# Optimization experiments

Measured on AMD Instinct MI355X. Metric: run time of the kernel, lower is better.

Reference implementation:

```python
import jax, jax.numpy as jnp
import numpy as np

B, L1, L2, D1, D2, H, P = 32, 256, 64, 256, 256, 256, 128
I = D1 + D2  # gate / GRU input dim


def setup_inputs() -> dict:
    key = jax.random.key(0)
    ks = jax.random.split(key, 10)
    s = 0.05  # weight init scale
    return {
        "sequence1": jax.random.normal(ks[0], (B, L1, D1), jnp.float32),
        "sequence2": jax.random.normal(ks[1], (B, L2, D2), jnp.float32),
        "sequence1_mask": jnp.ones((B, L1), jnp.float32),
        "sequence2_mask": jnp.ones((B, L2), jnp.float32),
        "W1": jax.random.normal(ks[2], (D2, P), jnp.float32) * s,
        "W2": jax.random.normal(ks[3], (D1 + H, P), jnp.float32) * s,
        "v": jax.random.normal(ks[4], (P,), jnp.float32) * s,
        "Wg": jax.random.normal(ks[5], (I, I), jnp.float32) * s,
        "bg": jnp.zeros((I,), jnp.float32),
        "w_ih": jax.random.normal(ks[6], (3 * H, I), jnp.float32) * s,
        "w_hh": jax.random.normal(ks[7], (3 * H, H), jnp.float32) * s,
        "b_ih": jnp.zeros((3 * H,), jnp.float32),
        "b_hh": jnp.zeros((3 * H,), jnp.float32),
    }


def reference(sequence1, sequence2, sequence1_mask, sequence2_mask,
              W1, W2, v, Wg, bg, w_ih, w_hh, b_ih, b_hh):
    # Precompute sequence2 projection once: [B, L2, P]
    seq2_proj = jnp.einsum('bld,dp->blp', sequence2, W1)
    # Additive mask for softmax over L2
    neg = jnp.where(sequence2_mask > 0, 0.0, -1e9)  # [B, L2]
    xs = jnp.transpose(sequence1, (1, 0, 2))  # [L1, B, D1]

    def step(h, x_t):
        # attention: v^T tanh(W1*seq2_j + W2*[x_t; h])
        vec = jnp.concatenate([x_t, h], axis=-1)            # [B, D1+H]
        s = jnp.einsum('blp,p->bl',
                       jnp.tanh(seq2_proj + (vec @ W2)[:, None, :]), v) + neg
        w = jax.nn.softmax(s, axis=-1)                      # [B, L2]
        att = jnp.einsum('bl,bld->bd', w, sequence2)        # [B, D2]
        inp = jnp.concatenate([x_t, att], axis=-1)          # [B, I]
        # gated attention: sigmoid(Linear(inp)) * inp
        inp = jax.nn.sigmoid(inp @ Wg.T + bg) * inp
        # GRUCell (torch semantics)
        gi = inp @ w_ih.T + b_ih
        gh = h @ w_hh.T + b_hh
        ir, iz, inn = jnp.split(gi, 3, axis=-1)
        hr, hz, hn = jnp.split(gh, 3, axis=-1)
        r = jax.nn.sigmoid(ir + hr)
        z = jax.nn.sigmoid(iz + hz)
        n = jnp.tanh(inn + r * hn)
        h_new = (1.0 - z) * n + z * h
        return h_new, h_new

    h0 = jnp.zeros((sequence1.shape[0], w_hh.shape[1]), sequence1.dtype)
    _, hs = jax.lax.scan(step, h0, xs)                      # [L1, B, H]
    out = jnp.transpose(hs, (1, 0, 2)) * sequence1_mask[:, :, None]
    return out
```

## Files before the change

### kernel.cpp

```cpp
#include <hip/hip_runtime.h>

typedef _Float16 half2_v __attribute__((ext_vector_type(2)));
typedef unsigned int u32;

#define W2K_O    0
#define WHHP_O   16384
#define WIHP_O   114688
#define NPACKW   311296
#define S2P_B    1245184
#define S2T_B    1769472
#define M1_B     2818048
#define PROJX_B  4915200
#define GATEX_B  7012352
#define EXCH_B   15400960

#define SMEM_BYTES 156928

__device__ __forceinline__ float fdot2(half2_v a, half2_v b, float c) {
    return __builtin_amdgcn_fdot2(a, b, c, false);
}
__device__ __forceinline__ half2_v h2_of(u32 u) { return __builtin_bit_cast(half2_v, u); }
__device__ __forceinline__ u32 pack_h2(float a, float b) {
    half2_v r; r[0] = (_Float16)a; r[1] = (_Float16)b;
    return __builtin_bit_cast(u32, r);
}
__device__ __forceinline__ float dot4(uint4 w, uint4 a, float acc) {
    acc = fdot2(h2_of(w.x), h2_of(a.x), acc);
    acc = fdot2(h2_of(w.y), h2_of(a.y), acc);
    acc = fdot2(h2_of(w.z), h2_of(a.z), acc);
    acc = fdot2(h2_of(w.w), h2_of(a.w), acc);
    return acc;
}
__device__ __forceinline__ float fast_tanh(float x) {
    float e = __expf(2.0f * x);
    return 1.0f - 2.0f / (e + 1.0f);
}
__device__ __forceinline__ float fast_sigmoid(float x) {
    return 1.0f / (1.0f + __expf(-x));
}
__device__ __forceinline__ u32 aload(const u32* p) {
    return __hip_atomic_load(p, __ATOMIC_RELAXED, __HIP_MEMORY_SCOPE_AGENT);
}
__device__ __forceinline__ void astore(u32* p, u32 v) {
    __hip_atomic_store(p, v, __ATOMIC_RELAXED, __HIP_MEMORY_SCOPE_AGENT);
}
__device__ __forceinline__ u32 mkw(float x, u32 st) {
    unsigned short hb = __builtin_bit_cast(unsigned short, (_Float16)x);
    return (st << 16) | (u32)hb;
}
__device__ __forceinline__ float f16low(u32 v) {
    return (float)__builtin_bit_cast(_Float16, (unsigned short)(v & 0xFFFFu));
}

__global__ void prep_pack_w(const float* __restrict__ W2, const float* __restrict__ wih,
                            const float* __restrict__ whh, u32* __restrict__ ws_u) {
    int idx = blockIdx.x * 256 + threadIdx.x;
    if (idx >= NPACKW) return;
    float a, c;
    if (idx < WHHP_O) {
        int mm = idx >> 11, r = idx & 2047, p = r >> 4, kl = r & 15;
        int row = 256 + mm * 32 + 2 * kl;
        a = W2[row * 128 + p]; c = W2[(row + 1) * 128 + p];
    } else if (idx < WIHP_O) {
        int t2 = idx - WHHP_O, mm = t2 / 12288, r = t2 % 12288, o = r >> 7, k = r & 127;
        int row = (o >> 5) * 256 + mm * 32 + (o & 31);
        a = whh[row * 256 + 2 * k]; c = whh[row * 256 + 2 * k + 1];
    } else {
        int t2 = idx - WIHP_O, mm = t2 / 24576, r = t2 % 24576, o = r >> 8, k = r & 255;
        int row = (o >> 5) * 256 + mm * 32 + (o & 31);
        a = wih[row * 512 + 2 * k]; c = wih[row * 512 + 2 * k + 1];
    }
    ws_u[idx] = pack_h2(a, c);
}

__global__ void prep_s2p(const float* __restrict__ seq2, const float* __restrict__ W1,
                         _Float16* __restrict__ outh) {
    int idx = blockIdx.x * 256 + threadIdx.x;
    int p = idx & 127, j = (idx >> 7) & 63, b = idx >> 13;
    const float* s2 = seq2 + (b * 64 + j) * 256;
    float acc = 0.f;
    #pragma unroll 8
    for (int d = 0; d < 256; ++d) acc += s2[d] * W1[d * 128 + p];
    outh[idx] = (_Float16)acc;
}

__global__ void prep_s2T(const float* __restrict__ seq2, _Float16* __restrict__ dst) {
    int idx = blockIdx.x * 256 + threadIdx.x;
    int j = idx & 63, d = (idx >> 6) & 255, b = idx >> 14;
    dst[idx] = (_Float16)seq2[(b * 64 + j) * 256 + d];
}

__global__ void prep_m1(const float* __restrict__ Wg, const float* __restrict__ seq2,
                        _Float16* __restrict__ dst) {
    int idx = blockIdx.x * 256 + threadIdx.x;
    int j = idx & 63, o = (idx >> 6) & 511, b = idx >> 15;
    const float* wr = Wg + o * 512 + 256;
    const float* s2 = seq2 + (b * 64 + j) * 256;
    float acc = 0.f;
    #pragma unroll 8
    for (int d = 0; d < 256; ++d) acc += wr[d] * s2[d];
    dst[idx] = (_Float16)acc;
}

__global__ void prep_gemm(const float* __restrict__ A, const float* __restrict__ Bsrc,
                          int mode, _Float16* __restrict__ C, int N) {
    __shared__ float As[64][17];
    __shared__ float Bs[16][65];
    int r0 = blockIdx.x * 64, n0 = blockIdx.y * 64;
    int tid = threadIdx.x;
    int tr = tid >> 4, tc = tid & 15;
    float acc[4][4] = {};
    for (int k0 = 0; k0 < 256; k0 += 16) {
        #pragma unroll
        for (int i = 0; i < 4; ++i) {
            int rr = (tid >> 4) + i * 16, kk = tid & 15;
            As[rr][kk] = A[(r0 + rr) * 256 + k0 + kk];
        }
        #pragma unroll
        for (int i = 0; i < 4; ++i) {
            if (mode == 0) { int kk = (tid >> 6) + i * 4, nn = tid & 63; Bs[kk][nn] = Bsrc[(k0 + kk) * N + n0 + nn]; }
            else           { int nn = (tid >> 4) + i * 16, kk = tid & 15; Bs[kk][nn] = Bsrc[(n0 + nn) * 512 + k0 + kk]; }
        }
        __syncthreads();
        #pragma unroll
        for (int k = 0; k < 16; ++k)
            #pragma unroll
            for (int i = 0; i < 4; ++i)
                #pragma unroll
                for (int j = 0; j < 4; ++j)
                    acc[i][j] += As[tr * 4 + i][k] * Bs[k][tc * 4 + j];
        __syncthreads();
    }
    for (int i = 0; i < 4; ++i)
        for (int j = 0; j < 4; ++j)
            C[(size_t)(r0 + tr * 4 + i) * N + n0 + tc * 4 + j] = (_Float16)acc[i][j];
}

__global__ void __launch_bounds__(1024) match_rnn(
    const float* __restrict__ seq1, const float* __restrict__ mask1,
    const float* __restrict__ mask2, const float* __restrict__ v,
    const float* __restrict__ bg, const float* __restrict__ bih,
    const float* __restrict__ bhh, char* __restrict__ ws, float* __restrict__ out)
{
    const int m = blockIdx.x >> 5;
    const int b = blockIdx.x & 31;
    const int tid = threadIdx.x;

    extern __shared__ char smem[];
    u32* s_whh4 = (u32*)smem;
    u32* s_wih4 = s_whh4 + 12288;
    u32* s_w2k  = s_wih4 + 12288;
    unsigned short* s_s2p = (unsigned short*)(s_w2k + 2176);
    u32* s_m1u  = (u32*)(s_s2p + 9216);
    u32* s_s2Tu = s_m1u + 2112;
    float* s_php = (float*)(s_s2Tu + 2112);
    float* s_red = s_php + 1024;
    u32* s_h2u  = (u32*)(s_red + 896);
    u32* s_ip2a = s_h2u + 160;
    u32* s_ip2b = s_ip2a + 160;
    float* s_projh = (float*)(s_ip2b + 160);
    float* s_projx = s_projh + 128;
    float* s_v   = s_projx + 128;
    float* s_w   = s_v + 128;
    float* s_neg = s_w + 64;
    float* s_gx  = s_neg + 64;
    float* s_xc  = s_gx + 64;
    float* s_bg  = s_xc + 64;
    float* s_sg  = s_bg + 64;
    float* s_attl = s_sg + 64;
    float* s_bih = s_attl + 64;
    float* s_bhh = s_bih + 96;
    float* s_gh  = s_bhh + 96;
    float* s_hf  = s_gh + 96;
    u32* s_hloc  = (u32*)(s_hf + 32);
    float* s_m1v = (float*)(s_hloc + 16);

    unsigned short* s_h2h  = (unsigned short*)s_h2u;
    unsigned short* s_ip2ah = (unsigned short*)s_ip2a;
    unsigned short* s_ip2bh = (unsigned short*)s_ip2b;

    const u32* wsrc = (const u32*)ws;

    for (int i = tid; i < 12288; i += 1024) {
        int o = i >> 7, k = i & 127, u = k >> 2;
        int du4 = ((o >> 3) * 256) + ((u & 3) * 64) + (((o & 7) << 3) | (u >> 2));
        s_whh4[du4 * 4 + (k & 3)] = wsrc[WHHP_O + m * 12288 + i];
    }
    for (int i = tid; i < 12288; i += 1024) {
        int o = i >> 7, k = i & 127, u = k >> 2;
        int du4 = ((o >> 3) * 256) + ((u & 3) * 64) + (((o & 7) << 3) | (u >> 2));
        s_wih4[du4 * 4 + (k & 3)] = wsrc[WIHP_O + m * 24576 + o * 256 + k];
    }
    for (int i = tid; i < 2048; i += 1024) {
        int p = i >> 4, kl = i & 15;
        s_w2k[p * 17 + kl] = wsrc[W2K_O + m * 2048 + i];
    }
    {
        const u32* s2src = wsrc + (S2P_B / 4) + b * 4096;
        for (int i = tid; i < 4096; i += 1024) {
            int j = i >> 6, kk = i & 63;
            ((u32*)s_s2p)[j * 72 + kk] = s2src[i];
        }
        const u32* m1src = wsrc + (M1_B / 4) + (b * 512 + m * 64) * 32;
        for (int i = tid; i < 2048; i += 1024) {
            int o = i >> 5, jw = i & 31;
            s_m1u[o * 33 + jw] = m1src[i];
        }
        if (m >= 4) {
            const u32* stsrc = wsrc + (S2T_B / 4) + (b * 256 + (m - 4) * 64) * 32;
            for (int i = tid; i < 2048; i += 1024) {
                int dd = i >> 5, jw = i & 31;
                s_s2Tu[dd * 33 + jw] = stsrc[i];
            }
        }
    }
    if (tid < 128) s_v[tid] = v[tid];
    if (tid < 64) { s_neg[tid] = (mask2[b * 64 + tid] > 0.f) ? 0.f : -1e9f; s_bg[tid] = bg[m * 64 + tid]; }
    if (tid < 96) {
        int row = (tid >> 5) * 256 + m * 32 + (tid & 31);
        s_bih[tid] = bih[row]; s_bhh[tid] = bhh[row];
    }
    if (tid < 32) s_hf[tid] = 0.f;

    uint4 wiA = {}, wiB = {}, wiC = {}, wiD = {};
    const int oAD = ((tid >> 6) << 3) + ((tid & 63) >> 3);
    const int ksAD = tid & 7;
    if (tid < 768) {
        const uint4* wip = (const uint4*)(wsrc + WIHP_O + m * 24576 + oAD * 256 + 128 + ksAD * 16);
        wiA = wip[0]; wiB = wip[1]; wiC = wip[2]; wiD = wip[3];
    }

    u32* exch = (u32*)(ws + EXCH_B) + b * 2048;
    const u32* g_projx = (const u32*)(ws + PROJX_B);
    const u32* g_gatex = (const u32*)(ws + GATEX_B);

    int dead = 0;
    __syncthreads();

    for (int t = 0; t < 256; ++t) {
        const u32 st = (u32)(t + 1);
        float4 xv = {};
        u32 pxv = 0, gxv = 0; float mkv = 0.f;
        if (tid >= 896 && tid < 912) {
            if (m < 4)
                xv = ((const float4*)(seq1 + (size_t)(b * 256 + t) * 256 + m * 64))[tid - 896];
        } else if (tid >= 912 && tid < 976)
            pxv = g_projx[(b * 256 + t) * 64 + (tid - 912)];
        else if (tid >= 976 && tid < 1008)
            gxv = g_gatex[(b * 256 + t) * 256 + m * 32 + (tid - 976)];
        else if (tid == 1008)
            mkv = mask1[b * 256 + t];

        if (t > 0) {
            u32 v1, v2;
            const bool p2 = tid < 256;
            const u32 stp = (u32)t;
            if (!dead) {
                int sp = 0;
                for (;;) {
                    v1 = aload(exch + tid);
                    v2 = p2 ? aload(exch + 1024 + tid) : (stp << 16);
                    bool ok = ((v1 >> 16) == stp) && ((v2 >> 16) == stp);
                    if (__all((int)ok)) break;
                    __builtin_amdgcn_s_sleep(1);
                    if (++sp > (1 << 17)) { dead = 1; break; }
                }
            } else { v1 = aload(exch + tid); v2 = p2 ? aload(exch + 1024 + tid) : 0; }
            { int mm = tid >> 7, p = tid & 127; s_php[p * 8 + mm] = f16low(v1); }
            if (p2) {
                int k = tid;
                int pos = ((k >> 5) * 20 + ((k >> 1) & 15)) * 2 + (k & 1);
                s_h2h[pos] = (unsigned short)(v2 & 0xFFFFu);
            }
        } else {
            if (tid < 160) s_h2u[tid] = 0u;
        }
        __syncthreads();

        if (tid < 768) {
            const uint4* wbase = (const uint4*)s_whh4 + (tid >> 6) * 256;
            float acc = 0.f;
            #pragma unroll
            for (int c = 0; c < 4; ++c) {
                uint4 wv = wbase[c * 64 + (tid & 63)];
                uint4 av = *(const uint4*)&s_h2u[ksAD * 20 + c * 4];
                acc = dot4(wv, av, acc);
            }
            s_red[oAD * 9 + ksAD] = acc;
        } else if (tid < 896) {
            int p = tid - 768;
            float a = 0.f;
            if (t > 0) {
                #pragma unroll
                for (int mm = 0; mm < 8; ++mm) a += s_php[p * 8 + mm];
            }
            s_projh[p] = a;
        } else if (tid < 912) {
            int q = tid - 896;
            s_xc[4 * q] = xv.x; s_xc[4 * q + 1] = xv.y; s_xc[4 * q + 2] = xv.z; s_xc[4 * q + 3] = xv.w;
        } else if (tid < 976) {
            half2_v h = h2_of(pxv); int i = tid - 912;
            s_projx[2 * i] = (float)h[0]; s_projx[2 * i + 1] = (float)h[1];
        } else if (tid < 1008) {
            half2_v h = h2_of(gxv); int i = tid - 976;
            s_gx[2 * i] = (float)h[0]; s_gx[2 * i + 1] = (float)h[1];
        } else if (tid == 1008) s_m1v[0] = mkv;
        __syncthreads();

        if (tid < 96) {
            float a = s_bhh[tid];
            #pragma unroll
            for (int k = 0; k < 8; ++k) a += s_red[tid * 9 + k];
            s_gh[tid] = a;
        }
        {
            int j = tid >> 4, pk = tid & 15, p0 = pk * 8;
            uint4 sv = *(const uint4*)&s_s2p[j * 144 + p0];
            const u32* su = (const u32*)&sv;
            float acc = 0.f;
            #pragma unroll
            for (int q = 0; q < 4; ++q) {
                half2_v h = h2_of(su[q]);
                int p = p0 + 2 * q;
                float a0 = (float)h[0] + s_projx[p] + s_projh[p];
                float a1 = (float)h[1] + s_projx[p + 1] + s_projh[p + 1];
                acc += fast_tanh(a0) * s_v[p];
                acc += fast_tanh(a1) * s_v[p + 1];
            }
            acc += __shfl_down(acc, 8, 16);
            acc += __shfl_down(acc, 4, 16);
            acc += __shfl_down(acc, 2, 16);
            acc += __shfl_down(acc, 1, 16);
            if (pk == 0) s_w[j] = acc + s_neg[j];
        }
        __syncthreads();
        if (tid < 64) {
            float sc = s_w[tid], mx = sc;
            #pragma unroll
            for (int off = 32; off > 0; off >>= 1) mx = fmaxf(mx, __shfl_xor(mx, off));
            float e = __expf(sc - mx), s = e;
            #pragma unroll
            for (int off = 32; off > 0; off >>= 1) s += __shfl_xor(s, off);
            s_w[tid] = e / s;
        }
        __syncthreads();

        if (tid < 512) {
            int o = tid >> 3, q = tid & 7;
            float acc = 0.f;
            #pragma unroll
            for (int c = 0; c < 4; ++c) {
                half2_v h = h2_of(s_m1u[o * 33 + q * 4 + c]);
                int j0 = (q * 4 + c) * 2;
                acc += (float)h[0] * s_w[j0] + (float)h[1] * s_w[j0 + 1];
            }
            acc += __shfl_down(acc, 4, 8);
            acc += __shfl_down(acc, 2, 8);
            acc += __shfl_down(acc, 1, 8);
            if (q == 0) s_sg[o] = fast_sigmoid(acc + s_gx[o] + s_bg[o]);
        } else {
            int dt = tid - 512, d = dt >> 3, q = dt & 7;
            float acc = 0.f;
            #pragma unroll
            for (int c = 0; c < 4; ++c) {
                half2_v h = h2_of(s_s2Tu[d * 33 + q * 4 + c]);
                int j0 = (q * 4 + c) * 2;
                acc += (float)h[0] * s_w[j0] + (float)h[1] * s_w[j0 + 1];
            }
            acc += __shfl_down(acc, 4, 8);
            acc += __shfl_down(acc, 2, 8);
            acc += __shfl_down(acc, 1, 8);
            if (q == 0) s_attl[d] = acc;
        }
        __syncthreads();

        if (tid < 64) {
            float inpv = (m < 4) ? s_xc[tid] : s_attl[tid];
            float ip = s_sg[tid] * inpv;
            astore(&exch[1280 + m * 64 + tid], mkw(ip, st));
        }
        if (tid < 512) {
            u32 vv;
            if (!dead) {
                int sp = 0;
                for (;;) {
                    vv = aload(exch + 1280 + tid);
                    if (__all((int)((vv >> 16) == st))) break;
                    __builtin_amdgcn_s_sleep(1);
                    if (++sp > (1 << 17)) { dead = 1; break; }
                }
            } else vv = aload(exch + 1280 + tid);
            int i = tid;
            if (i < 256) {
                int pos = ((i >> 5) * 20 + ((i >> 1) & 15)) * 2 + (i & 1);
                s_ip2ah[pos] = (unsigned short)(vv & 0xFFFFu);
            } else {
                int i2 = i - 256;
                int pos = ((i2 >> 5) * 20 + ((i2 >> 1) & 15)) * 2 + (i2 & 1);
                s_ip2bh[pos] = (unsigned short)(vv & 0xFFFFu);
            }
        }
        __syncthreads();

        if (tid < 768) {
            const uint4* wbase = (const uint4*)s_wih4 + (tid >> 6) * 256;
            float acc = 0.f;
            #pragma unroll
            for (int c = 0; c < 4; ++c) {
                uint4 wv = wbase[c * 64 + (tid & 63)];
                uint4 av = *(const uint4*)&s_ip2a[ksAD * 20 + c * 4];
                acc = dot4(wv, av, acc);
            }
            acc = dot4(wiA, *(const uint4*)&s_ip2b[ksAD * 20 + 0],  acc);
            acc = dot4(wiB, *(const uint4*)&s_ip2b[ksAD * 20 + 4],  acc);
            acc = dot4(wiC, *(const uint4*)&s_ip2b[ksAD * 20 + 8],  acc);
            acc = dot4(wiD, *(const uint4*)&s_ip2b[ksAD * 20 + 12], acc);
            s_red[oAD * 9 + ksAD] = acc;
        }
        __syncthreads();

        if (tid < 32) {
            int o = tid;
            float gr = s_bih[o], gz = s_bih[32 + o], gn = s_bih[64 + o];
            #pragma unroll
            for (int k = 0; k < 8; ++k) {
                gr += s_red[o * 9 + k];
                gz += s_red[(32 + o) * 9 + k];
                gn += s_red[(64 + o) * 9 + k];
            }
            float r_ = fast_sigmoid(gr + s_gh[o]);
            float z_ = fast_sigmoid(gz + s_gh[32 + o]);
            float n_ = fast_tanh(gn + r_ * s_gh[64 + o]);
            float hn = (1.f - z_) * n_ + z_ * s_hf[o];
            s_hf[o] = hn;
            out[(size_t)(b * 256 + t) * 256 + m * 32 + o] = hn * s_m1v[0];
            astore(&exch[1024 + m * 32 + o], mkw(hn, st));
            float nb = __shfl_down(hn, 1);
            if (!(o & 1)) s_hloc[o >> 1] = pack_h2(hn, nb);
        }
        __syncthreads();

        if (tid < 512) {
            int p = tid >> 2, kc = tid & 3;
            float a = 0.f;
            #pragma unroll
            for (int cc = 0; cc < 4; ++cc)
                a = fdot2(h2_of(s_w2k[p * 17 + kc * 4 + cc]), h2_of(s_hloc[kc * 4 + cc]), a);
            a += __shfl_down(a, 2, 4);
            a += __shfl_down(a, 1, 4);
            if (kc == 0) astore(&exch[m * 128 + p], mkw(a, st));
        }
    }
}

extern "C" void kernel_launch(void* const* d_in, const int* in_sizes, int n_in,
                              void* d_out, int out_size, void* d_ws, size_t ws_size,
                              hipStream_t stream) {
    const float* seq1  = (const float*)d_in[0];
    const float* seq2  = (const float*)d_in[1];
    const float* mask1 = (const float*)d_in[2];
    const float* mask2 = (const float*)d_in[3];
    const float* W1    = (const float*)d_in[4];
    const float* W2    = (const float*)d_in[5];
    const float* v     = (const float*)d_in[6];
    const float* Wg    = (const float*)d_in[7];
    const float* bg    = (const float*)d_in[8];
    const float* wih   = (const float*)d_in[9];
    const float* whh   = (const float*)d_in[10];
    const float* bih   = (const float*)d_in[11];
    const float* bhh   = (const float*)d_in[12];

    char* ws = (char*)d_ws;

    (void)hipFuncSetAttribute(reinterpret_cast<const void*>(match_rnn),
                              hipFuncAttributeMaxDynamicSharedMemorySize, SMEM_BYTES);

    prep_pack_w<<<dim3((NPACKW + 255) / 256), dim3(256), 0, stream>>>(W2, wih, whh, (u32*)ws);
    prep_s2p<<<dim3(1024), dim3(256), 0, stream>>>(seq2, W1, (_Float16*)(ws + S2P_B));
    prep_s2T<<<dim3(2048), dim3(256), 0, stream>>>(seq2, (_Float16*)(ws + S2T_B));
    prep_m1<<<dim3(4096), dim3(256), 0, stream>>>(Wg, seq2, (_Float16*)(ws + M1_B));
    prep_gemm<<<dim3(128, 2), dim3(256), 0, stream>>>(seq1, W2, 0, (_Float16*)(ws + PROJX_B), 128);
    prep_gemm<<<dim3(128, 8), dim3(256), 0, stream>>>(seq1, Wg, 1, (_Float16*)(ws + GATEX_B), 512);
    (void)hipMemsetAsync(ws + EXCH_B, 0, 262144, stream);
    match_rnn<<<dim3(256), dim3(1024), SMEM_BYTES, stream>>>(seq1, mask1, mask2, v, bg, bih, bhh, ws, (float*)d_out);
}
```

Measured before the change: 1.815 ms.

## Replace shared-memory reductions with wave shuffles and drop per-step barriers

Partial sums for the hidden projection, W_hh and W_ih products are now reduced with intra-wave shuffles instead of being written to shared memory and summed in a separate phase. The softmax and gate/attention stages are merged into one phase that broadcasts weights with shuffles, removing two __syncthreads per timestep. The exchange layout for projh partials becomes p*8+m so the eight contributions sit in adjacent lanes, and spin-waits now poll a few times before sleeping to cut inter-block handoff latency. Shared memory shrinks, and s_s2Tu is zero-filled for blocks that do not load it because every block now reads it. The cost is more shuffle instructions and busier spinning on the exchange buffer.

```diff
diff --git a/kernel.cpp b/kernel.cpp
--- a/kernel.cpp
+++ b/kernel.cpp
@@ -14,7 +14,7 @@
 #define GATEX_B  7012352
 #define EXCH_B   15400960
 
-#define SMEM_BYTES 156928
+#define SMEM_BYTES 148816
 
 __device__ __forceinline__ float fdot2(half2_v a, half2_v b, float c) {
     return __builtin_amdgcn_fdot2(a, b, c, false);
@@ -150,12 +150,12 @@
     u32* s_whh4 = (u32*)smem;
     u32* s_wih4 = s_whh4 + 12288;
     u32* s_w2k  = s_wih4 + 12288;
-    unsigned short* s_s2p = (unsigned short*)(s_w2k + 2176);
-    u32* s_m1u  = (u32*)(s_s2p + 9216);
+    u32* s_s2pU = s_w2k + 2176;
+    u32* s_m1u  = s_s2pU + 4608;
     u32* s_s2Tu = s_m1u + 2112;
-    float* s_php = (float*)(s_s2Tu + 2112);
-    float* s_red = s_php + 1024;
-    u32* s_h2u  = (u32*)(s_red + 896);
+    float* s_redA = (float*)(s_s2Tu + 2112);
+    float* s_redD = s_redA + 96;
+    u32* s_h2u  = (u32*)(s_redD + 96);
     u32* s_ip2a = s_h2u + 160;
     u32* s_ip2b = s_ip2a + 160;
     float* s_projh = (float*)(s_ip2b + 160);
@@ -166,15 +166,13 @@
     float* s_gx  = s_neg + 64;
     float* s_xc  = s_gx + 64;
     float* s_bg  = s_xc + 64;
-    float* s_sg  = s_bg + 64;
-    float* s_attl = s_sg + 64;
-    float* s_bih = s_attl + 64;
+    float* s_bih = s_bg + 64;
     float* s_bhh = s_bih + 96;
-    float* s_gh  = s_bhh + 96;
-    float* s_hf  = s_gh + 96;
+    float* s_hf  = s_bhh + 96;
     u32* s_hloc  = (u32*)(s_hf + 32);
     float* s_m1v = (float*)(s_hloc + 16);
 
+    unsigned short* s_s2p  = (unsigned short*)s_s2pU;
     unsigned short* s_h2h  = (unsigned short*)s_h2u;
     unsigned short* s_ip2ah = (unsigned short*)s_ip2a;
     unsigned short* s_ip2bh = (unsigned short*)s_ip2b;
@@ -199,7 +197,7 @@
         const u32* s2src = wsrc + (S2P_B / 4) + b * 4096;
         for (int i = tid; i < 4096; i += 1024) {
             int j = i >> 6, kk = i & 63;
-            ((u32*)s_s2p)[j * 72 + kk] = s2src[i];
+            s_s2pU[j * 72 + kk] = s2src[i];
         }
         const u32* m1src = wsrc + (M1_B / 4) + (b * 512 + m * 64) * 32;
         for (int i = tid; i < 2048; i += 1024) {
@@ -212,6 +210,8 @@
                 int dd = i >> 5, jw = i & 31;
                 s_s2Tu[dd * 33 + jw] = stsrc[i];
             }
+        } else {
+            for (int i = tid; i < 2112; i += 1024) s_s2Tu[i] = 0u;
         }
     }
     if (tid < 128) s_v[tid] = v[tid];
@@ -262,11 +262,15 @@
                     v2 = p2 ? aload(exch + 1024 + tid) : (stp << 16);
                     bool ok = ((v1 >> 16) == stp) && ((v2 >> 16) == stp);
                     if (__all((int)ok)) break;
-                    __builtin_amdgcn_s_sleep(1);
-                    if (++sp > (1 << 17)) { dead = 1; break; }
+                    if (++sp > 16) __builtin_amdgcn_s_sleep(1);
+                    if (sp > (1 << 17)) { dead = 1; break; }
                 }
             } else { v1 = aload(exch + tid); v2 = p2 ? aload(exch + 1024 + tid) : 0; }
-            { int mm = tid >> 7, p = tid & 127; s_php[p * 8 + mm] = f16low(v1); }
+            float ph = f16low(v1);
+            ph += __shfl_down(ph, 4, 8);
+            ph += __shfl_down(ph, 2, 8);
+            ph += __shfl_down(ph, 1, 8);
+            if ((tid & 7) == 0) s_projh[tid >> 3] = ph;
             if (p2) {
                 int k = tid;
                 int pos = ((k >> 5) * 20 + ((k >> 1) & 15)) * 2 + (k & 1);
@@ -274,6 +278,7 @@
             }
         } else {
             if (tid < 160) s_h2u[tid] = 0u;
+            if (tid < 128) s_projh[tid] = 0.f;
         }
         __syncthreads();
 
@@ -282,37 +287,26 @@
             float acc = 0.f;
             #pragma unroll
             for (int c = 0; c < 4; ++c) {
-                uint4 wv = wbase[c * 64 + (tid & 63)];
+                uint4 wv4 = wbase[c * 64 + (tid & 63)];
                 uint4 av = *(const uint4*)&s_h2u[ksAD * 20 + c * 4];
-                acc = dot4(wv, av, acc);
-            }
-            s_red[oAD * 9 + ksAD] = acc;
-        } else if (tid < 896) {
-            int p = tid - 768;
-            float a = 0.f;
-            if (t > 0) {
-                #pragma unroll
-                for (int mm = 0; mm < 8; ++mm) a += s_php[p * 8 + mm];
-            }
-            s_projh[p] = a;
-        } else if (tid < 912) {
+                acc = dot4(wv4, av, acc);
+            }
+            acc += __shfl_down(acc, 4, 8);
+            acc += __shfl_down(acc, 2, 8);
+            acc += __shfl_down(acc, 1, 8);
+            if (ksAD == 0) s_redA[oAD] = acc + s_bhh[oAD];
+        } else if (tid >= 896 && tid < 912) {
             int q = tid - 896;
             s_xc[4 * q] = xv.x; s_xc[4 * q + 1] = xv.y; s_xc[4 * q + 2] = xv.z; s_xc[4 * q + 3] = xv.w;
-        } else if (tid < 976) {
+        } else if (tid >= 912 && tid < 976) {
             half2_v h = h2_of(pxv); int i = tid - 912;
             s_projx[2 * i] = (float)h[0]; s_projx[2 * i + 1] = (float)h[1];
-        } else if (tid < 1008) {
+        } else if (tid >= 976 && tid < 1008) {
             half2_v h = h2_of(gxv); int i = tid - 976;
             s_gx[2 * i] = (float)h[0]; s_gx[2 * i + 1] = (float)h[1];
         } else if (tid == 1008) s_m1v[0] = mkv;
         __syncthreads();
 
-        if (tid < 96) {
-            float a = s_bhh[tid];
-            #pragma unroll
-            for (int k = 0; k < 8; ++k) a += s_red[tid * 9 + k];
-            s_gh[tid] = a;
-        }
         {
             int j = tid >> 4, pk = tid & 15, p0 = pk * 8;
             uint4 sv = *(const uint4*)&s_s2p[j * 144 + p0];
@@ -334,50 +328,37 @@
             if (pk == 0) s_w[j] = acc + s_neg[j];
         }
         __syncthreads();
-        if (tid < 64) {
-            float sc = s_w[tid], mx = sc;
+
+        float wv;
+        {
+            float sc = s_w[tid & 63];
+            float mx = sc;
             #pragma unroll
             for (int off = 32; off > 0; off >>= 1) mx = fmaxf(mx, __shfl_xor(mx, off));
-            float e = __expf(sc - mx), s = e;
-            #pragma unroll
-            for (int off = 32; off > 0; off >>= 1) s += __shfl_xor(s, off);
-            s_w[tid] = e / s;
-        }
-        __syncthreads();
-
-        if (tid < 512) {
-            int o = tid >> 3, q = tid & 7;
+            float e = __expf(sc - mx), ssum = e;
+            #pragma unroll
+            for (int off = 32; off > 0; off >>= 1) ssum += __shfl_xor(ssum, off);
+            wv = e / ssum;
+        }
+        {
+            int o = tid >> 4, r = tid & 15, q = r & 7;
+            const u32* src = (r >= 8) ? &s_s2Tu[o * 33] : &s_m1u[o * 33];
             float acc = 0.f;
             #pragma unroll
             for (int c = 0; c < 4; ++c) {
-                half2_v h = h2_of(s_m1u[o * 33 + q * 4 + c]);
+                half2_v h = h2_of(src[q * 4 + c]);
                 int j0 = (q * 4 + c) * 2;
-                acc += (float)h[0] * s_w[j0] + (float)h[1] * s_w[j0 + 1];
+                acc += (float)h[0] * __shfl(wv, j0) + (float)h[1] * __shfl(wv, j0 + 1);
             }
             acc += __shfl_down(acc, 4, 8);
             acc += __shfl_down(acc, 2, 8);
             acc += __shfl_down(acc, 1, 8);
-            if (q == 0) s_sg[o] = fast_sigmoid(acc + s_gx[o] + s_bg[o]);
-        } else {
-            int dt = tid - 512, d = dt >> 3, q = dt & 7;
-            float acc = 0.f;
-            #pragma unroll
-            for (int c = 0; c < 4; ++c) {
-                half2_v h = h2_of(s_s2Tu[d * 33 + q * 4 + c]);
-                int j0 = (q * 4 + c) * 2;
-                acc += (float)h[0] * s_w[j0] + (float)h[1] * s_w[j0 + 1];
-            }
-            acc += __shfl_down(acc, 4, 8);
-            acc += __shfl_down(acc, 2, 8);
-            acc += __shfl_down(acc, 1, 8);
-            if (q == 0) s_attl[d] = acc;
-        }
-        __syncthreads();
-
-        if (tid < 64) {
-            float inpv = (m < 4) ? s_xc[tid] : s_attl[tid];
-            float ip = s_sg[tid] * inpv;
-            astore(&exch[1280 + m * 64 + tid], mkw(ip, st));
+            float attv = __shfl(acc, ((tid & 63) + 8) & 63);
+            if (r == 0) {
+                float g = acc + s_gx[o] + s_bg[o];
+                float inpv = (m < 4) ? s_xc[o] : attv;
+                astore(&exch[1280 + m * 64 + o], mkw(fast_sigmoid(g) * inpv, st));
+            }
         }
         if (tid < 512) {
             u32 vv;
@@ -386,8 +367,8 @@
                 for (;;) {
                     vv = aload(exch + 1280 + tid);
                     if (__all((int)((vv >> 16) == st))) break;
-                    __builtin_amdgcn_s_sleep(1);
-                    if (++sp > (1 << 17)) { dead = 1; break; }
+                    if (++sp > 16) __builtin_amdgcn_s_sleep(1);
+                    if (sp > (1 << 17)) { dead = 1; break; }
                 }
             } else vv = aload(exch + 1280 + tid);
             int i = tid;
@@ -407,30 +388,26 @@
             float acc = 0.f;
             #pragma unroll
             for (int c = 0; c < 4; ++c) {
-                uint4 wv = wbase[c * 64 + (tid & 63)];
+                uint4 wv4 = wbase[c * 64 + (tid & 63)];
                 uint4 av = *(const uint4*)&s_ip2a[ksAD * 20 + c * 4];
-                acc = dot4(wv, av, acc);
+                acc = dot4(wv4, av, acc);
             }
             acc = dot4(wiA, *(const uint4*)&s_ip2b[ksAD * 20 + 0],  acc);
             acc = dot4(wiB, *(const uint4*)&s_ip2b[ksAD * 20 + 4],  acc);
             acc = dot4(wiC, *(const uint4*)&s_ip2b[ksAD * 20 + 8],  acc);
             acc = dot4(wiD, *(const uint4*)&s_ip2b[ksAD * 20 + 12], acc);
-            s_red[oAD * 9 + ksAD] = acc;
+            acc += __shfl_down(acc, 4, 8);
+            acc += __shfl_down(acc, 2, 8);
+            acc += __shfl_down(acc, 1, 8);
+            if (ksAD == 0) s_redD[oAD] = acc + s_bih[oAD];
         }
         __syncthreads();
 
         if (tid < 32) {
             int o = tid;
-            float gr = s_bih[o], gz = s_bih[32 + o], gn = s_bih[64 + o];
-            #pragma unroll
-            for (int k = 0; k < 8; ++k) {
-                gr += s_red[o * 9 + k];
-                gz += s_red[(32 + o) * 9 + k];
-                gn += s_red[(64 + o) * 9 + k];
-            }
-            float r_ = fast_sigmoid(gr + s_gh[o]);
-            float z_ = fast_sigmoid(gz + s_gh[32 + o]);
-            float n_ = fast_tanh(gn + r_ * s_gh[64 + o]);
+            float r_ = fast_sigmoid(s_redD[o] + s_redA[o]);
+            float z_ = fast_sigmoid(s_redD[32 + o] + s_redA[32 + o]);
+            float n_ = fast_tanh(s_redD[64 + o] + r_ * s_redA[64 + o]);
             float hn = (1.f - z_) * n_ + z_ * s_hf[o];
             s_hf[o] = hn;
             out[(size_t)(b * 256 + t) * 256 + m * 32 + o] = hn * s_m1v[0];
@@ -448,7 +425,7 @@
                 a = fdot2(h2_of(s_w2k[p * 17 + kc * 4 + cc]), h2_of(s_hloc[kc * 4 + cc]), a);
             a += __shfl_down(a, 2, 4);
             a += __shfl_down(a, 1, 4);
-            if (kc == 0) astore(&exch[m * 128 + p], mkw(a, st));
+            if (kc == 0) astore(&exch[p * 8 + m], mkw(a, st));
         }
     }
 }
```

New measurement: 2.114 ms. +16.5%, slower.
